# Performance work log

Hardware: AMD Instinct MI355X
Metric: run time of the kernel (lower is better)

The kernel has to match this reference:

```python
import jax, jax.numpy as jnp
import numpy as np

N = 100_000      # total nodes in batched graph
NE = 800_000     # total edges
G = 1_000        # number of graphs in batch
V_DIM = 128      # node feat dim (== H_DIM, required by GRUCell usage)
E_DIM = 64       # edge feat dim
H_DIM = 128      # hidden dim
K_HEAD = 4       # multi-scale interaction heads


def _leaky(x):
    return jnp.where(x >= 0, x, 0.1 * x)


def _gru_cell(x, h, Wih, Whh, bih, bhh):
    # torch nn.GRUCell math; Wih/Whh stored as [in, 3*h] with (r,z,n) chunk order
    gi = x @ Wih + bih
    gh = h @ Whh + bhh
    ir, iz, inn = jnp.split(gi, 3, axis=-1)
    hr, hz, hn = jnp.split(gh, 3, axis=-1)
    r = jax.nn.sigmoid(ir + hr)
    z = jax.nn.sigmoid(iz + hz)
    n = jnp.tanh(inn + r * hn)
    return (1.0 - z) * n + z * h


def setup_inputs() -> dict:
    key = jax.random.key(0)
    ks = iter(jax.random.split(key, 48))
    def rn(shape, scale=0.05):
        return (jax.random.normal(next(ks), shape) * scale).astype(jnp.float32)
    inp = {}
    inp["v"] = rn((N, V_DIM), 1.0)
    inp["e"] = rn((NE, E_DIM), 1.0)
    inp["s"] = rn((G, V_DIM), 1.0)
    inp["edge_src"] = jax.random.randint(next(ks), (NE,), 0, N)
    inp["edge_dst"] = jax.random.randint(next(ks), (NE,), 0, N)
    inp["node_graph"] = jnp.repeat(jnp.arange(G), N // G)  # sorted segment ids
    # top-level linears (stored [in, out])
    inp["A_w"] = rn((V_DIM, H_DIM)); inp["A_b"] = rn((H_DIM,))
    inp["mA_w"] = rn((K_HEAD, V_DIM, H_DIM)); inp["mA_b"] = rn((K_HEAD, H_DIM))
    inp["mB_w"] = rn((K_HEAD, V_DIM, H_DIM)); inp["mB_b"] = rn((K_HEAD, H_DIM))
    inp["mC_w"] = rn((K_HEAD, H_DIM)); inp["mC_b"] = rn((K_HEAD,))
    inp["mD_w"] = rn((K_HEAD, V_DIM, H_DIM)); inp["mD_b"] = rn((K_HEAD, H_DIM))
    inp["B_w"] = rn((H_DIM * K_HEAD, H_DIM)); inp["B_b"] = rn((H_DIM,))
    inp["C_w"] = rn((V_DIM, H_DIM)); inp["C_b"] = rn((H_DIM,))
    inp["K_w"] = rn((E_DIM, H_DIM)); inp["K_b"] = rn((H_DIM,))
    inp["E_w"] = rn((H_DIM + V_DIM, H_DIM)); inp["E_b"] = rn((H_DIM,))
    for pfx in ("gm", "gs"):
        inp[pfx + "_A_w"] = rn((H_DIM, H_DIM)); inp[pfx + "_A_b"] = rn((H_DIM,))
        inp[pfx + "_B_w"] = rn((H_DIM, H_DIM)); inp[pfx + "_B_b"] = rn((H_DIM,))
        inp[pfx + "_Wih"] = rn((H_DIM, 3 * H_DIM)); inp[pfx + "_Whh"] = rn((H_DIM, 3 * H_DIM))
        inp[pfx + "_bih"] = rn((3 * H_DIM,)); inp[pfx + "_bhh"] = rn((3 * H_DIM,))
    return inp


def reference(v, e, s, edge_src, edge_dst, node_graph,
              A_w, A_b, mA_w, mA_b, mB_w, mB_b, mC_w, mC_b, mD_w, mD_b,
              B_w, B_b, C_w, C_b, K_w, K_b, E_w, E_b,
              gm_A_w, gm_A_b, gm_B_w, gm_B_b, gm_Wih, gm_Whh, gm_bih, gm_bhh,
              gs_A_w, gs_A_b, gs_B_w, gs_B_b, gs_Wih, gs_Whh, gs_bih, gs_bhh):
    # super -> super
    s2s = jnp.tanh(s @ A_w + A_b)                                       # [G,H]
    # multi-head node->super attention pooling (Multi_scale_interaction)
    d_node = jnp.tanh(jnp.einsum('nv,kvh->knh', v, mA_w) + mA_b[:, None, :])     # [K,N,H]
    d_super = jnp.tanh(jnp.einsum('gv,kvh->kgh', s, mB_w) + mB_b[:, None, :])    # [K,G,H]
    a = jnp.einsum('knh,kh->nk', d_node * d_super[:, node_graph, :], mC_w) + mC_b[None, :]  # [N,K]
    a_max = jax.ops.segment_max(a, node_graph, num_segments=G, indices_are_sorted=True)
    a_exp = jnp.exp(a - a_max[node_graph])
    denom = jax.ops.segment_sum(a_exp, node_graph, num_segments=G, indices_are_sorted=True)
    attn = a_exp / denom[node_graph]                                    # per-graph softmax, [N,K]
    d_v = jnp.einsum('nv,kvh->nkh', v, mD_w) + mD_b[None, :, :]         # [N,K,H]
    pooled = jax.ops.segment_sum(d_v * attn[:, :, None], node_graph, num_segments=G,
                                 indices_are_sorted=True)               # [G,K,H]
    m2s = jnp.tanh(pooled.reshape(G, K_HEAD * H_DIM) @ B_w + B_b)       # [G,H]
    # super -> node broadcast
    s2m = jnp.tanh(s @ C_w + C_b)[node_graph]                           # [N,H]
    # edge-wise message: leaky_relu(K(e) * v_src) summed into destination node
    ve = _leaky((e @ K_w + K_b) * v[edge_src])                          # [E,H]
    sve = jax.ops.segment_sum(ve, edge_dst, num_segments=N)             # [N,H]
    m2m = _leaky(jnp.concatenate([sve, v], axis=1) @ E_w + E_b)         # [N,H]
    # adaptive GRU gate: node update
    z_m = jax.nn.sigmoid(m2m @ gm_A_w + gm_A_b + s2m @ gm_B_w + gm_B_b)
    h_m = z_m * s2m + (1.0 - z_m) * m2m
    update_v = _gru_cell(v, h_m, gm_Wih, gm_Whh, gm_bih, gm_bhh)
    # adaptive GRU gate: supernode update
    z_s = jax.nn.sigmoid(s2s @ gs_A_w + gs_A_b + m2s @ gs_B_w + gs_B_b)
    h_s = z_s * m2s + (1.0 - z_s) * s2s
    update_s = _gru_cell(s, h_s, gs_Wih, gs_Whh, gs_bih, gs_bhh)
    return (update_v, update_s)
```

## Files before the change

kernel.cpp:

```cpp
#include <hip/hip_runtime.h>

#define NN   100000
#define NEDG 800000
#define NG   1000
#define HD   128
#define EDIM 64

typedef unsigned short u16;
typedef __bf16 bf16x8 __attribute__((ext_vector_type(8)));
typedef float f32x4 __attribute__((ext_vector_type(4)));
typedef u16 u16x8 __attribute__((ext_vector_type(8)));
typedef unsigned u32x4 __attribute__((ext_vector_type(4)));

#define MFMA16(a, b, c) __builtin_amdgcn_mfma_f32_16x16x32_bf16(a, b, c, 0, 0, 0)

#define WS_E    0
#define WS_GA   4096
#define WS_WIH  6144
#define WS_WHH  12288
#define WS_MA0  18432
#define WS_KW   26624
#define WS_LANES 27648

#define BF(base, NTT, ks, nt, lane) \
    (*(const bf16x8*)(wsw + (size_t)((base) + (((ks) * (NTT) + (nt)) * 64 + (lane))) * 8))

__device__ __forceinline__ float sigmoidf_(float x) { return 1.0f / (1.0f + __expf(-x)); }
__device__ __forceinline__ float tanhf_(float x) {
    float ax = fabsf(x);
    float e  = __expf(-2.0f * ax);
    float t  = (1.0f - e) / (1.0f + e);
    return copysignf(t, x);
}
__device__ __forceinline__ float leaky_(float x) { return x >= 0.f ? x : 0.1f * x; }
__device__ __forceinline__ u16 f2bf(float x) {
    union { float f; unsigned u; } c; c.f = x;
    unsigned r = c.u + 0x7FFF + ((c.u >> 16) & 1);
    return (u16)(r >> 16);
}
__device__ __forceinline__ float bfbits2f(unsigned hw) {
    union { unsigned u; float f; } c; c.u = hw << 16; return c.f;
}
__device__ __forceinline__ unsigned pack2bf(float lo, float hi) {
    return (unsigned)f2bf(lo) | ((unsigned)f2bf(hi) << 16);
}
__device__ __forceinline__ bf16x8 mk8(const float* __restrict__ p) {
    float4 a = *(const float4*)p;
    float4 b = *(const float4*)(p + 4);
    union { u32x4 u; bf16x8 v; } c;
    c.u[0] = pack2bf(a.x, a.y);
    c.u[1] = pack2bf(a.z, a.w);
    c.u[2] = pack2bf(b.x, b.y);
    c.u[3] = pack2bf(b.z, b.w);
    return c.v;
}

__device__ __forceinline__ void stg4(u16* lds, int P, int r, int c0, float4 v4) {
    int byteoff = (c0 << 1) ^ ((r & 7) << 4);
    u16* p = lds + r * P + (byteoff >> 1);
    p[0] = f2bf(v4.x); p[1] = f2bf(v4.y); p[2] = f2bf(v4.z); p[3] = f2bf(v4.w);
}
__device__ __forceinline__ void stg1(u16* lds, int P, int r, int c, u16 val) {
    int byteoff = (c << 1) ^ ((r & 7) << 4);
    lds[r * P + (byteoff >> 1)] = val;
}
__device__ __forceinline__ bf16x8 ldA(const u16* lds, int P, int r, int ks, int hi) {
    int byteoff = (ks * 64 + (hi << 4)) ^ ((r & 7) << 4);
    return *(const bf16x8*)(lds + r * P + (byteoff >> 1));
}

__global__ __launch_bounds__(256) void wconv(
    const float* __restrict__ E_w, const float* __restrict__ gmA_w,
    const float* __restrict__ Wih, const float* __restrict__ Whh,
    const float* __restrict__ mA_w, const float* __restrict__ K_w,
    u16* __restrict__ dst)
{
    int t = blockIdx.x * 256 + threadIdx.x;
    if (t >= WS_LANES) return;
    const float* W; int N; int local;
    if (t < 4096)       { W = E_w;  N = 128; local = t; }
    else if (t < 6144)  { W = gmA_w; N = 128; local = t - 4096; }
    else if (t < 12288) { W = Wih;  N = 384; local = t - 6144; }
    else if (t < 18432) { W = Whh;  N = 384; local = t - 12288; }
    else if (t < 26624) { int k = (t - 18432) >> 11; W = mA_w + k * 128 * 128; N = 128; local = (t - 18432) & 2047; }
    else                { W = K_w;  N = 128; local = t - 26624; }
    int lane = local & 63;
    int fid  = local >> 6;
    int NT = N >> 4;
    int ks = fid / NT, nt = fid - ks * NT;
    int krow = ks * 32 + ((lane >> 4) << 3);
    int col  = nt * 16 + (lane & 15);
    u16* d = dst + (size_t)t * 8;
    #pragma unroll
    for (int j = 0; j < 8; j++) d[j] = f2bf(W[(size_t)(krow + j) * N + col]);
}

__global__ __launch_bounds__(256) void k_hist(const int* __restrict__ edst, int* __restrict__ cnt) {
    int i = blockIdx.x * 256 + threadIdx.x;
    if (i < NEDG) atomicAdd(&cnt[edst[i]], 1);
}

__global__ __launch_bounds__(256) void k_scan1(const int* __restrict__ cnt,
                                               int* __restrict__ excl, int* __restrict__ bsum) {
    __shared__ int sd[256];
    int t = threadIdx.x, b = blockIdx.x;
    int base = b * 1024 + t * 4;
    int v0 = (base + 0 < NN) ? cnt[base + 0] : 0;
    int v1 = (base + 1 < NN) ? cnt[base + 1] : 0;
    int v2 = (base + 2 < NN) ? cnt[base + 2] : 0;
    int v3 = (base + 3 < NN) ? cnt[base + 3] : 0;
    int s = v0 + v1 + v2 + v3;
    sd[t] = s;
    __syncthreads();
    for (int off = 1; off < 256; off <<= 1) {
        int x = (t >= off) ? sd[t - off] : 0;
        __syncthreads();
        sd[t] += x;
        __syncthreads();
    }
    int incl = sd[t];
    int ex = incl - s;
    if (base + 0 < NN) excl[base + 0] = ex;
    if (base + 1 < NN) excl[base + 1] = ex + v0;
    if (base + 2 < NN) excl[base + 2] = ex + v0 + v1;
    if (base + 3 < NN) excl[base + 3] = ex + v0 + v1 + v2;
    if (t == 255) bsum[b] = incl;
}

#define NSCB 98
__global__ void k_scan2(int* __restrict__ bsum) {
    if (threadIdx.x == 0 && blockIdx.x == 0) {
        int run = 0;
        for (int i = 0; i < NSCB; i++) { int t = bsum[i]; bsum[i] = run; run += t; }
    }
}

__global__ __launch_bounds__(256) void k_scan3(const int* __restrict__ excl,
                                               const int* __restrict__ bsum,
                                               int* __restrict__ start, int* __restrict__ rowptr) {
    int i = blockIdx.x * 256 + threadIdx.x;
    if (i < NN) {
        int sv = excl[i] + bsum[i >> 10];
        start[i] = sv;
        rowptr[i] = sv;
    }
    if (i == NN) rowptr[NN] = NEDG;
}

__global__ __launch_bounds__(256) void k_scatter(const int* __restrict__ edst,
                                                 int* __restrict__ start,
                                                 int* __restrict__ perm,
                                                 int* __restrict__ outpos) {
    int i = blockIdx.x * 256 + threadIdx.x;
    if (i < NEDG) {
        int pos = atomicAdd(&start[edst[i]], 1);
        perm[pos] = i;
        outpos[i] = pos;
    }
}

__global__ __launch_bounds__(128) void k1_graph(
    const float* __restrict__ s,
    const float* __restrict__ A_w, const float* __restrict__ A_b,
    const float* __restrict__ mB_w, const float* __restrict__ mB_b,
    const float* __restrict__ mC_w,
    const float* __restrict__ C_w, const float* __restrict__ C_b,
    const float* __restrict__ gmB_w, const float* __restrict__ gmA_b, const float* __restrict__ gmB_b,
    float* __restrict__ s2s, float* __restrict__ wkg,
    float* __restrict__ s2m_tab, float* __restrict__ t2)
{
    __shared__ float sm[HD];
    __shared__ float sm2[HD];
    const int g = blockIdx.x, t = threadIdx.x;
    sm[t] = s[g * HD + t];
    __syncthreads();
    {
        float a = 0.f;
        #pragma unroll 8
        for (int i = 0; i < HD; i++) a = fmaf(sm[i], A_w[i * HD + t], a);
        s2s[g * HD + t] = tanhf_(a + A_b[t]);
    }
    for (int k = 0; k < 4; k++) {
        float a = 0.f;
        const float* W = mB_w + k * HD * HD;
        #pragma unroll 8
        for (int i = 0; i < HD; i++) a = fmaf(sm[i], W[i * HD + t], a);
        float d = tanhf_(a + mB_b[k * HD + t]);
        wkg[(k * NG + g) * HD + t] = d * mC_w[k * HD + t];
    }
    float s2m;
    {
        float a = 0.f;
        #pragma unroll 8
        for (int i = 0; i < HD; i++) a = fmaf(sm[i], C_w[i * HD + t], a);
        s2m = tanhf_(a + C_b[t]);
        s2m_tab[g * HD + t] = s2m;
    }
    sm2[t] = s2m;
    __syncthreads();
    {
        float a = 0.f;
        #pragma unroll 8
        for (int i = 0; i < HD; i++) a = fmaf(sm2[i], gmB_w[i * HD + t], a);
        t2[g * HD + t] = a + gmA_b[t] + gmB_b[t];
    }
}

__global__ __launch_bounds__(256) void k2_ascore(
    const float* __restrict__ v, const int* __restrict__ ngr,
    const u16* __restrict__ wsw,
    const float* __restrict__ mA_b, const float* __restrict__ mC_b,
    const float* __restrict__ wkg,
    float* __restrict__ aexp, float* __restrict__ denom)
{
    __shared__ u16 VT[64 * 128];
    const int tid = threadIdx.x;
    const int n0 = blockIdx.x * 64;
    #pragma unroll
    for (int l = 0; l < 8; l++) {
        int i = tid + 256 * l;
        int r = i >> 5, c0 = (i & 31) << 2;
        int node = n0 + r;
        float4 vv = (node < NN) ? *(const float4*)(v + (size_t)node * HD + c0)
                                : make_float4(0.f, 0.f, 0.f, 0.f);
        stg4(VT, 128, r, c0, vv);
    }
    __syncthreads();
    const int lane = tid & 63, w = tid >> 6;
    const int l15 = lane & 15, hi = lane >> 4;
    const int rbase = w * 16;
    bf16x8 av[4];
    #pragma unroll
    for (int ks = 0; ks < 4; ks++) av[ks] = ldA(VT, 128, rbase + l15, ks, hi);
    int gq[4], nodeq[4];
    #pragma unroll
    for (int q = 0; q < 4; q++) {
        int nd = n0 + rbase + hi * 4 + q;
        nodeq[q] = nd;
        gq[q] = ngr[min(nd, NN - 1)];
    }
    for (int k = 0; k < 4; k++) {
        float rs[4] = {0.f, 0.f, 0.f, 0.f};
        const float* bias = mA_b + k * HD;
        #pragma unroll
        for (int nt = 0; nt < 8; nt++) {
            f32x4 acc = {0.f, 0.f, 0.f, 0.f};
            #pragma unroll
            for (int ks = 0; ks < 4; ks++)
                acc = MFMA16(av[ks], BF(WS_MA0 + k * 2048, 8, ks, nt, lane), acc);
            int col = nt * 16 + l15;
            float bb = bias[col];
            #pragma unroll
            for (int q = 0; q < 4; q++)
                rs[q] += tanhf_(acc[q] + bb) * wkg[((size_t)k * NG + gq[q]) * HD + col];
        }
        #pragma unroll
        for (int q = 0; q < 4; q++) {
            float x = rs[q];
            x += __shfl_xor(x, 1); x += __shfl_xor(x, 2);
            x += __shfl_xor(x, 4); x += __shfl_xor(x, 8);
            if (l15 == 0 && nodeq[q] < NN) {
                float ev = __expf(x + mC_b[k]);
                aexp[(size_t)nodeq[q] * 4 + k] = ev;
                atomicAdd(&denom[gq[q] * 4 + k], ev);
            }
        }
    }
}

__global__ __launch_bounds__(256) void k3a_edge(
    const float* __restrict__ e, const float* __restrict__ v,
    const int* __restrict__ esrc, const int* __restrict__ outpos,
    const u16* __restrict__ wsw, const float* __restrict__ K_b,
    u16* __restrict__ vesrt)
{
    __shared__ u16 ET[64 * 64];
    __shared__ u16 OUT[64 * 128];
    __shared__ int posa[64];
    const int tid = threadIdx.x;
    const int e0 = blockIdx.x * 64;
    if (tid < 64) posa[tid] = outpos[e0 + tid];
    #pragma unroll
    for (int l = 0; l < 4; l++) {
        int i = tid + 256 * l;
        int r = i >> 4, c0 = (i & 15) << 2;
        float4 ev4 = *(const float4*)(e + (size_t)(e0 + r) * EDIM + c0);
        stg4(ET, 64, r, c0, ev4);
    }
    __syncthreads();
    const int lane = tid & 63, w = tid >> 6;
    const int l15 = lane & 15, hi = lane >> 4;
    const int rbase = w * 16;
    bf16x8 ae[2];
    #pragma unroll
    for (int ks = 0; ks < 2; ks++) ae[ks] = ldA(ET, 64, rbase + l15, ks, hi);
    int sq[4];
    #pragma unroll
    for (int q = 0; q < 4; q++) sq[q] = esrc[e0 + rbase + hi * 4 + q];
    #pragma unroll
    for (int nt = 0; nt < 8; nt++) {
        f32x4 acc = {0.f, 0.f, 0.f, 0.f};
        acc = MFMA16(ae[0], BF(WS_KW, 8, 0, nt, lane), acc);
        acc = MFMA16(ae[1], BF(WS_KW, 8, 1, nt, lane), acc);
        int col = nt * 16 + l15;
        float kb = K_b[col];
        #pragma unroll
        for (int q = 0; q < 4; q++) {
            float val = leaky_((acc[q] + kb) * v[(size_t)sq[q] * HD + col]);
            stg1(OUT, 128, rbase + hi * 4 + q, col, f2bf(val));
        }
    }
    __syncthreads();
    #pragma unroll
    for (int l = 0; l < 4; l++) {
        int i = tid + 256 * l;
        int r = i >> 4, seg = i & 15;
        int segp = seg ^ (r & 7);
        u16x8 val = *(const u16x8*)&OUT[r * 128 + segp * 8];
        *(u16x8*)(vesrt + (size_t)posa[r] * HD + ((segp ^ (r & 7)) * 8)) = val;
    }
}

__global__ __launch_bounds__(256) void k3b_segsum(
    const u16* __restrict__ vesrt, const int* __restrict__ rowptr,
    float* __restrict__ sve)
{
    const int wid = threadIdx.x >> 6, lane = threadIdx.x & 63;
    const int n = blockIdx.x * 4 + wid;
    if (n >= NN) return;
    const int r0 = rowptr[n], r1 = rowptr[n + 1];
    const unsigned* base = (const unsigned*)vesrt;
    float a0 = 0.f, a1 = 0.f;
    int r = r0;
    for (; r + 4 <= r1; r += 4) {
        unsigned x0 = base[(size_t)(r + 0) * 64 + lane];
        unsigned x1 = base[(size_t)(r + 1) * 64 + lane];
        unsigned x2 = base[(size_t)(r + 2) * 64 + lane];
        unsigned x3 = base[(size_t)(r + 3) * 64 + lane];
        a0 += bfbits2f(x0 & 0xffff) + bfbits2f(x1 & 0xffff) + bfbits2f(x2 & 0xffff) + bfbits2f(x3 & 0xffff);
        a1 += bfbits2f(x0 >> 16) + bfbits2f(x1 >> 16) + bfbits2f(x2 >> 16) + bfbits2f(x3 >> 16);
    }
    for (; r < r1; r++) {
        unsigned x = base[(size_t)r * 64 + lane];
        a0 += bfbits2f(x & 0xffff);
        a1 += bfbits2f(x >> 16);
    }
    *(float2*)(sve + (size_t)n * HD + lane * 2) = make_float2(a0, a1);
}

__global__ __launch_bounds__(256) void k3_edge_sorted(
    const float* __restrict__ e, const float* __restrict__ v,
    const int* __restrict__ esrc, const int* __restrict__ edst,
    const int* __restrict__ perm,
    const u16* __restrict__ wsw, const float* __restrict__ K_b,
    float* __restrict__ sve)
{
    __shared__ u16 ET[64 * 64];
    __shared__ int pid[64];
    const int tid = threadIdx.x;
    const int e0 = blockIdx.x * 64;
    if (tid < 64) pid[tid] = perm[e0 + tid];
    __syncthreads();
    #pragma unroll
    for (int l = 0; l < 4; l++) {
        int i = tid + 256 * l;
        int r = i >> 4, c0 = (i & 15) << 2;
        float4 ev4 = *(const float4*)(e + (size_t)pid[r] * EDIM + c0);
        stg4(ET, 64, r, c0, ev4);
    }
    __syncthreads();
    const int lane = tid & 63, w = tid >> 6;
    const int l15 = lane & 15, hi = lane >> 4;
    const int rbase = w * 16;
    bf16x8 ae[2];
    #pragma unroll
    for (int ks = 0; ks < 2; ks++) ae[ks] = ldA(ET, 64, rbase + l15, ks, hi);
    int sq[4], dq[4];
    #pragma unroll
    for (int q = 0; q < 4; q++) {
        int ei = pid[rbase + hi * 4 + q];
        sq[q] = esrc[ei]; dq[q] = edst[ei];
    }
    #pragma unroll
    for (int nt = 0; nt < 8; nt++) {
        f32x4 acc = {0.f, 0.f, 0.f, 0.f};
        acc = MFMA16(ae[0], BF(WS_KW, 8, 0, nt, lane), acc);
        acc = MFMA16(ae[1], BF(WS_KW, 8, 1, nt, lane), acc);
        int col = nt * 16 + l15;
        float kb = K_b[col];
        float vals[4];
        #pragma unroll
        for (int q = 0; q < 4; q++)
            vals[q] = leaky_((acc[q] + kb) * v[(size_t)sq[q] * HD + col]);
        float a = vals[0];
        #pragma unroll
        for (int q = 1; q < 4; q++) {
            if (dq[q] == dq[q - 1]) a += vals[q];
            else { atomicAdd(&sve[(size_t)dq[q - 1] * HD + col], a); a = vals[q]; }
        }
        atomicAdd(&sve[(size_t)dq[3] * HD + col], a);
    }
}

__global__ __launch_bounds__(256) void k3_edge_unsorted(
    const float* __restrict__ e, const float* __restrict__ v,
    const int* __restrict__ esrc, const int* __restrict__ edst,
    const u16* __restrict__ wsw, const float* __restrict__ K_b,
    float* __restrict__ sve)
{
    __shared__ u16 ET[64 * 64];
    const int tid = threadIdx.x;
    const int e0 = blockIdx.x * 64;
    #pragma unroll
    for (int l = 0; l < 4; l++) {
        int i = tid + 256 * l;
        int r = i >> 4, c0 = (i & 15) << 2;
        float4 ev4 = *(const float4*)(e + (size_t)(e0 + r) * EDIM + c0);
        stg4(ET, 64, r, c0, ev4);
    }
    __syncthreads();
    const int lane = tid & 63, w = tid >> 6;
    const int l15 = lane & 15, hi = lane >> 4;
    const int rbase = w * 16;
    bf16x8 ae[2];
    #pragma unroll
    for (int ks = 0; ks < 2; ks++) ae[ks] = ldA(ET, 64, rbase + l15, ks, hi);
    int sq[4], dq[4];
    #pragma unroll
    for (int q = 0; q < 4; q++) {
        int ei = e0 + rbase + hi * 4 + q;
        sq[q] = esrc[ei]; dq[q] = edst[ei];
    }
    #pragma unroll
    for (int nt = 0; nt < 8; nt++) {
        f32x4 acc = {0.f, 0.f, 0.f, 0.f};
        acc = MFMA16(ae[0], BF(WS_KW, 8, 0, nt, lane), acc);
        acc = MFMA16(ae[1], BF(WS_KW, 8, 1, nt, lane), acc);
        int col = nt * 16 + l15;
        float kb = K_b[col];
        #pragma unroll
        for (int q = 0; q < 4; q++) {
            float val = leaky_((acc[q] + kb) * v[(size_t)sq[q] * HD + col]);
            atomicAdd(&sve[(size_t)dq[q] * HD + col], val);
        }
    }
}

__global__ __launch_bounds__(256) void k4_vbar(
    const float* __restrict__ v, const int* __restrict__ ngr,
    const float* __restrict__ aexp, const float* __restrict__ denom,
    float* __restrict__ vbar)
{
    const int tid = threadIdx.x;
    const int d = tid & 127;
    const int hf = tid >> 7;
    const int n0 = blockIdx.x * 32 + hf * 16;
    int gcur = -1;
    float a0 = 0.f, a1 = 0.f, a2 = 0.f, a3 = 0.f;
    float4 rd = make_float4(0.f, 0.f, 0.f, 0.f);
    for (int nd = 0; nd < 16; nd++) {
        int n = n0 + nd;
        int g = ngr[n];
        if (g != gcur) {
            if (gcur >= 0) {
                atomicAdd(&vbar[(gcur * 4 + 0) * HD + d], a0);
                atomicAdd(&vbar[(gcur * 4 + 1) * HD + d], a1);
                atomicAdd(&vbar[(gcur * 4 + 2) * HD + d], a2);
                atomicAdd(&vbar[(gcur * 4 + 3) * HD + d], a3);
                a0 = a1 = a2 = a3 = 0.f;
            }
            float4 dn = *(const float4*)&denom[g * 4];
            rd = make_float4(1.f / dn.x, 1.f / dn.y, 1.f / dn.z, 1.f / dn.w);
            gcur = g;
        }
        float4 ae = *(const float4*)&aexp[n * 4];
        float vv = v[(size_t)n * HD + d];
        a0 = fmaf(ae.x * rd.x, vv, a0);
        a1 = fmaf(ae.y * rd.y, vv, a1);
        a2 = fmaf(ae.z * rd.z, vv, a2);
        a3 = fmaf(ae.w * rd.w, vv, a3);
    }
    atomicAdd(&vbar[(gcur * 4 + 0) * HD + d], a0);
    atomicAdd(&vbar[(gcur * 4 + 1) * HD + d], a1);
    atomicAdd(&vbar[(gcur * 4 + 2) * HD + d], a2);
    atomicAdd(&vbar[(gcur * 4 + 3) * HD + d], a3);
}

__global__ __launch_bounds__(128) void k5_super(
    const float* __restrict__ s, const float* __restrict__ vbar,
    const float* __restrict__ mD_w, const float* __restrict__ mD_b,
    const float* __restrict__ B_w, const float* __restrict__ B_b,
    const float* __restrict__ s2s,
    const float* __restrict__ gsA_w, const float* __restrict__ gsA_b,
    const float* __restrict__ gsB_w, const float* __restrict__ gsB_b,
    const float* __restrict__ gsWih, const float* __restrict__ gsWhh,
    const float* __restrict__ gsbih, const float* __restrict__ gsbhh,
    float* __restrict__ out_s)
{
    __shared__ float vb[4 * HD];
    __shared__ float p[4 * HD];
    __shared__ float m2s_l[HD];
    __shared__ float s2s_l[HD];
    __shared__ float hs_l[HD];
    __shared__ float srow[HD];
    const int g = blockIdx.x, t = threadIdx.x;
    #pragma unroll
    for (int l = 0; l < 4; l++) vb[t + HD * l] = vbar[(size_t)g * 4 * HD + t + HD * l];
    srow[t]  = s[g * HD + t];
    s2s_l[t] = s2s[g * HD + t];
    __syncthreads();
    for (int k = 0; k < 4; k++) {
        float a = 0.f;
        const float* W = mD_w + k * HD * HD;
        #pragma unroll 8
        for (int i = 0; i < HD; i++) a = fmaf(vb[k * HD + i], W[i * HD + t], a);
        p[k * HD + t] = a + mD_b[k * HD + t];
    }
    __syncthreads();
    float m2s;
    {
        float a = 0.f;
        #pragma unroll 8
        for (int j = 0; j < 4 * HD; j++) a = fmaf(p[j], B_w[j * HD + t], a);
        m2s = tanhf_(a + B_b[t]);
        m2s_l[t] = m2s;
    }
    __syncthreads();
    float hs;
    {
        float za = 0.f, zb = 0.f;
        #pragma unroll 8
        for (int i = 0; i < HD; i++) {
            za = fmaf(s2s_l[i], gsA_w[i * HD + t], za);
            zb = fmaf(m2s_l[i], gsB_w[i * HD + t], zb);
        }
        float z = sigmoidf_(za + gsA_b[t] + zb + gsB_b[t]);
        hs = z * m2s + (1.f - z) * s2s_l[t];
        hs_l[t] = hs;
    }
    __syncthreads();
    float gi0 = 0.f, gh0 = 0.f, gi1 = 0.f, gh1 = 0.f, gi2 = 0.f, gh2 = 0.f;
    #pragma unroll 4
    for (int i = 0; i < HD; i++) {
        float sv = srow[i], hv = hs_l[i];
        gi0 = fmaf(sv, gsWih[i * 384 + t], gi0);
        gh0 = fmaf(hv, gsWhh[i * 384 + t], gh0);
        gi1 = fmaf(sv, gsWih[i * 384 + 128 + t], gi1);
        gh1 = fmaf(hv, gsWhh[i * 384 + 128 + t], gh1);
        gi2 = fmaf(sv, gsWih[i * 384 + 256 + t], gi2);
        gh2 = fmaf(hv, gsWhh[i * 384 + 256 + t], gh2);
    }
    float r  = sigmoidf_(gi0 + gsbih[t] + gh0 + gsbhh[t]);
    float z2 = sigmoidf_(gi1 + gsbih[128 + t] + gh1 + gsbhh[128 + t]);
    float nn = tanhf_(gi2 + gsbih[256 + t] + r * (gh2 + gsbhh[256 + t]));
    out_s[g * HD + t] = (1.f - z2) * nn + z2 * hs;
}

__global__ __launch_bounds__(256) void k6_node(
    const float* __restrict__ v, const int* __restrict__ ngr,
    const float* __restrict__ sve, const u16* __restrict__ wsw,
    const float* __restrict__ E_b,
    const float* __restrict__ s2m_tab, const float* __restrict__ t2,
    const float* __restrict__ bih, const float* __restrict__ bhh,
    float* __restrict__ out_v)
{
    __shared__ u16 TT[4][16 * 128];
    const int tid = threadIdx.x;
    const int lane = tid & 63, w = tid >> 6;
    const int l15 = lane & 15, hi = lane >> 4;
    const int n0 = blockIdx.x * 64 + w * 16;
    u16* T = TT[w];
    const int arow = min(n0 + l15, NN - 1);
    bf16x8 av[4], ax[4];
    #pragma unroll
    for (int ks = 0; ks < 4; ks++) {
        av[ks] = mk8(v   + (size_t)arow * HD + ks * 32 + hi * 8);
        ax[ks] = mk8(sve + (size_t)arow * HD + ks * 32 + hi * 8);
    }
    int gq[4], nodeq[4];
    #pragma unroll
    for (int q = 0; q < 4; q++) {
        int nd = n0 + hi * 4 + q;
        nodeq[q] = nd;
        gq[q] = ngr[min(nd, NN - 1)];
    }
    f32x4 hmf[8];
    #pragma unroll
    for (int nt = 0; nt < 8; nt++) {
        f32x4 acc = {0.f, 0.f, 0.f, 0.f};
        #pragma unroll
        for (int ks = 0; ks < 4; ks++) acc = MFMA16(ax[ks], BF(WS_E, 8, ks, nt, lane), acc);
        #pragma unroll
        for (int ks = 0; ks < 4; ks++) acc = MFMA16(av[ks], BF(WS_E, 8, 4 + ks, nt, lane), acc);
        float eb = E_b[nt * 16 + l15];
        #pragma unroll
        for (int q = 0; q < 4; q++) hmf[nt][q] = leaky_(acc[q] + eb);
    }
    #pragma unroll
    for (int nt = 0; nt < 8; nt++) {
        int col = nt * 16 + l15;
        #pragma unroll
        for (int q = 0; q < 4; q++) stg1(T, 128, hi * 4 + q, col, f2bf(hmf[nt][q]));
    }
    bf16x8 am[4];
    #pragma unroll
    for (int ks = 0; ks < 4; ks++) am[ks] = ldA(T, 128, l15, ks, hi);
    #pragma unroll
    for (int nt = 0; nt < 8; nt++) {
        f32x4 acc = {0.f, 0.f, 0.f, 0.f};
        #pragma unroll
        for (int ks = 0; ks < 4; ks++) acc = MFMA16(am[ks], BF(WS_GA, 8, ks, nt, lane), acc);
        int col = nt * 16 + l15;
        #pragma unroll
        for (int q = 0; q < 4; q++) {
            int g = gq[q];
            float z  = sigmoidf_(acc[q] + t2[(size_t)g * HD + col]);
            hmf[nt][q] = z * s2m_tab[(size_t)g * HD + col] + (1.f - z) * hmf[nt][q];
        }
    }
    #pragma unroll
    for (int nt = 0; nt < 8; nt++) {
        int col = nt * 16 + l15;
        #pragma unroll
        for (int q = 0; q < 4; q++) stg1(T, 128, hi * 4 + q, col, f2bf(hmf[nt][q]));
    }
    bf16x8 ah[4];
    #pragma unroll
    for (int ks = 0; ks < 4; ks++) ah[ks] = ldA(T, 128, l15, ks, hi);
    #pragma unroll
    for (int nt = 0; nt < 8; nt++) {
        f32x4 air = {0.f,0.f,0.f,0.f}, aiz = {0.f,0.f,0.f,0.f}, ain = {0.f,0.f,0.f,0.f};
        f32x4 ahr = {0.f,0.f,0.f,0.f}, ahz = {0.f,0.f,0.f,0.f}, ahn = {0.f,0.f,0.f,0.f};
        #pragma unroll
        for (int ks = 0; ks < 4; ks++) {
            air = MFMA16(av[ks], BF(WS_WIH, 24, ks, nt,      lane), air);
            ahr = MFMA16(ah[ks], BF(WS_WHH, 24, ks, nt,      lane), ahr);
            aiz = MFMA16(av[ks], BF(WS_WIH, 24, ks, nt + 8,  lane), aiz);
            ahz = MFMA16(ah[ks], BF(WS_WHH, 24, ks, nt + 8,  lane), ahz);
            ain = MFMA16(av[ks], BF(WS_WIH, 24, ks, nt + 16, lane), ain);
            ahn = MFMA16(ah[ks], BF(WS_WHH, 24, ks, nt + 16, lane), ahn);
        }
        int col = nt * 16 + l15;
        float br  = bih[col] + bhh[col];
        float bz  = bih[HD + col] + bhh[HD + col];
        float bi3 = bih[2 * HD + col];
        float bh3 = bhh[2 * HD + col];
        #pragma unroll
        for (int q = 0; q < 4; q++) {
            float r   = sigmoidf_(air[q] + ahr[q] + br);
            float z   = sigmoidf_(aiz[q] + ahz[q] + bz);
            float nnv = tanhf_(ain[q] + bi3 + r * (ahn[q] + bh3));
            if (nodeq[q] < NN)
                out_v[(size_t)nodeq[q] * HD + col] = (1.f - z) * nnv + z * hmf[nt][q];
        }
    }
}

extern "C" void kernel_launch(void* const* d_in, const int* in_sizes, int n_in,
                              void* d_out, int out_size, void* d_ws, size_t ws_size,
                              hipStream_t stream)
{
    const float* v    = (const float*)d_in[0];
    const float* e    = (const float*)d_in[1];
    const float* s    = (const float*)d_in[2];
    const int*   esrc = (const int*)d_in[3];
    const int*   edst = (const int*)d_in[4];
    const int*   ngr  = (const int*)d_in[5];
    const float* A_w  = (const float*)d_in[6];
    const float* A_b  = (const float*)d_in[7];
    const float* mA_w = (const float*)d_in[8];
    const float* mA_b = (const float*)d_in[9];
    const float* mB_w = (const float*)d_in[10];
    const float* mB_b = (const float*)d_in[11];
    const float* mC_w = (const float*)d_in[12];
    const float* mC_b = (const float*)d_in[13];
    const float* mD_w = (const float*)d_in[14];
    const float* mD_b = (const float*)d_in[15];
    const float* B_w  = (const float*)d_in[16];
    const float* B_b  = (const float*)d_in[17];
    const float* C_w  = (const float*)d_in[18];
    const float* C_b  = (const float*)d_in[19];
    const float* K_w  = (const float*)d_in[20];
    const float* K_b  = (const float*)d_in[21];
    const float* E_w  = (const float*)d_in[22];
    const float* E_b  = (const float*)d_in[23];
    const float* gmA_w = (const float*)d_in[24];
    const float* gmA_b = (const float*)d_in[25];
    const float* gmB_w = (const float*)d_in[26];
    const float* gmB_b = (const float*)d_in[27];
    const float* gmWih = (const float*)d_in[28];
    const float* gmWhh = (const float*)d_in[29];
    const float* gmbih = (const float*)d_in[30];
    const float* gmbhh = (const float*)d_in[31];
    const float* gsA_w = (const float*)d_in[32];
    const float* gsA_b = (const float*)d_in[33];
    const float* gsB_w = (const float*)d_in[34];
    const float* gsB_b = (const float*)d_in[35];
    const float* gsWih = (const float*)d_in[36];
    const float* gsWhh = (const float*)d_in[37];
    const float* gsbih = (const float*)d_in[38];
    const float* gsbhh = (const float*)d_in[39];

    float* ws      = (float*)d_ws;
    float* sve     = ws;
    float* aexp    = sve + 12800000;
    float* denom   = aexp + 400000;
    float* wkg     = denom + 4000;
    float* s2s     = wkg + 512000;
    float* s2m_tab = s2s + 128000;
    float* t2      = s2m_tab + 128000;
    float* vbar    = t2 + 128000;
    u16*   wswz    = (u16*)(vbar + 512000);
    int*   isc     = (int*)(wswz + 221184);
    int*   cnt     = isc;
    int*   excl    = cnt + 100000;
    int*   bsum    = excl + 100000;
    int*   startp  = bsum + 128;
    int*   rowptr  = startp + 100000;
    int*   perm    = rowptr + 100032;
    int*   outpos  = perm + 800000;
    u16*   vesrt   = (u16*)(outpos + 800000);
    const size_t NEED_SORT = ((size_t)((int*)vesrt - (int*)d_ws)) * 4;
    const size_t NEED_FULL = NEED_SORT + (size_t)102400000 * 2;
    const bool do_sort = ws_size >= NEED_SORT;
    const bool do_full = ws_size >= NEED_FULL;

    hipMemsetAsync(denom, 0, (size_t)4000 * 4, stream);
    hipMemsetAsync(vbar, 0, (size_t)512000 * 4, stream);
    if (!do_full) hipMemsetAsync(sve, 0, (size_t)12800000 * 4, stream);

    float* out_v = (float*)d_out;
    float* out_s = out_v + (size_t)NN * HD;

    wconv<<<(WS_LANES + 255) / 256, 256, 0, stream>>>(E_w, gmA_w, gmWih, gmWhh, mA_w, K_w, wswz);
    k1_graph<<<NG, 128, 0, stream>>>(s, A_w, A_b, mB_w, mB_b, mC_w, C_w, C_b,
                                     gmB_w, gmA_b, gmB_b, s2s, wkg, s2m_tab, t2);
    if (do_sort) {
        hipMemsetAsync(cnt, 0, (size_t)100000 * 4, stream);
        k_hist<<<(NEDG + 255) / 256, 256, 0, stream>>>(edst, cnt);
        k_scan1<<<NSCB, 256, 0, stream>>>(cnt, excl, bsum);
        k_scan2<<<1, 64, 0, stream>>>(bsum);
        k_scan3<<<(NN + 256) / 256, 256, 0, stream>>>(excl, bsum, startp, rowptr);
        k_scatter<<<(NEDG + 255) / 256, 256, 0, stream>>>(edst, startp, perm, outpos);
    }
    k2_ascore<<<(NN + 63) / 64, 256, 0, stream>>>(v, ngr, wswz, mA_b, mC_b, wkg, aexp, denom);
    if (do_full) {
        k3a_edge<<<NEDG / 64, 256, 0, stream>>>(e, v, esrc, outpos, wswz, K_b, vesrt);
        k3b_segsum<<<(NN + 3) / 4, 256, 0, stream>>>(vesrt, rowptr, sve);
    } else if (do_sort) {
        k3_edge_sorted<<<NEDG / 64, 256, 0, stream>>>(e, v, esrc, edst, perm, wswz, K_b, sve);
    } else {
        k3_edge_unsorted<<<NEDG / 64, 256, 0, stream>>>(e, v, esrc, edst, wswz, K_b, sve);
    }
    k4_vbar<<<NN / 32, 256, 0, stream>>>(v, ngr, aexp, denom, vbar);
    k5_super<<<NG, 128, 0, stream>>>(s, vbar, mD_w, mD_b, B_w, B_b, s2s,
                                     gsA_w, gsA_b, gsB_w, gsB_b,
                                     gsWih, gsWhh, gsbih, gsbhh, out_s);
    k6_node<<<(NN + 63) / 64, 256, 0, stream>>>(v, ngr, sve, wswz, E_b, s2m_tab, t2,
                                                gmbih, gmbhh, out_v);
}
```

Baseline: 739.0 us.

## Fuse CSR segment-sum of edge messages into node GRU kernel

In the sorted-edge path, the per-node segment sum over bf16 edge messages now runs inside the node update kernel, which writes the sums straight into LDS as the MFMA A operand. This removes the separate segsum kernel and the fp32 sve round trip through global memory. The cost is that each wave loops serially over its 16 nodes, which may unbalance work and lengthen the node kernel. The node kernel is also moved earlier in the launch order, before vbar and the supernode kernel.

```diff
diff --git a/kernel.cpp b/kernel.cpp
--- a/kernel.cpp
+++ b/kernel.cpp
@@ -63,6 +63,10 @@
 __device__ __forceinline__ void stg1(u16* lds, int P, int r, int c, u16 val) {
     int byteoff = (c << 1) ^ ((r & 7) << 4);
     lds[r * P + (byteoff >> 1)] = val;
+}
+__device__ __forceinline__ void stgu32(u16* lds, int P, int r, int cpair, unsigned val) {
+    int byteoff = (cpair << 2) ^ ((r & 7) << 4);
+    *(unsigned*)(lds + r * P + (byteoff >> 1)) = val;
 }
 __device__ __forceinline__ bf16x8 ldA(const u16* lds, int P, int r, int ks, int hi) {
     int byteoff = (ks * 64 + (hi << 4)) ^ ((r & 7) << 4);
@@ -556,7 +560,131 @@
     out_s[g * HD + t] = (1.f - z2) * nn + z2 * hs;
 }
 
-__global__ __launch_bounds__(256) void k6_node(
+__global__ __launch_bounds__(256) void k6_fused(
+    const float* __restrict__ v, const int* __restrict__ ngr,
+    const u16* __restrict__ vesrt, const int* __restrict__ rowptr,
+    const u16* __restrict__ wsw,
+    const float* __restrict__ E_b,
+    const float* __restrict__ s2m_tab, const float* __restrict__ t2,
+    const float* __restrict__ bih, const float* __restrict__ bhh,
+    float* __restrict__ out_v)
+{
+    __shared__ u16 TT[4][16 * 128];
+    const int tid = threadIdx.x;
+    const int lane = tid & 63, w = tid >> 6;
+    const int l15 = lane & 15, hi = lane >> 4;
+    const int n0 = blockIdx.x * 64 + w * 16;
+    u16* T = TT[w];
+    const int arow = min(n0 + l15, NN - 1);
+    bf16x8 av[4];
+    #pragma unroll
+    for (int ks = 0; ks < 4; ks++) av[ks] = mk8(v + (size_t)arow * HD + ks * 32 + hi * 8);
+    const unsigned* vb = (const unsigned*)vesrt;
+    for (int i = 0; i < 16; i++) {
+        int n = min(n0 + i, NN - 1);
+        int r0 = rowptr[n], r1 = rowptr[n + 1];
+        float a0 = 0.f, a1 = 0.f;
+        int r = r0;
+        for (; r + 4 <= r1; r += 4) {
+            unsigned x0 = vb[(size_t)(r + 0) * 64 + lane];
+            unsigned x1 = vb[(size_t)(r + 1) * 64 + lane];
+            unsigned x2 = vb[(size_t)(r + 2) * 64 + lane];
+            unsigned x3 = vb[(size_t)(r + 3) * 64 + lane];
+            a0 += bfbits2f(x0 & 0xffff) + bfbits2f(x1 & 0xffff) + bfbits2f(x2 & 0xffff) + bfbits2f(x3 & 0xffff);
+            a1 += bfbits2f(x0 >> 16) + bfbits2f(x1 >> 16) + bfbits2f(x2 >> 16) + bfbits2f(x3 >> 16);
+        }
+        for (; r < r1; r++) {
+            unsigned x = vb[(size_t)r * 64 + lane];
+            a0 += bfbits2f(x & 0xffff);
+            a1 += bfbits2f(x >> 16);
+        }
+        stgu32(T, 128, i, lane, pack2bf(a0, a1));
+    }
+    bf16x8 ax[4];
+    #pragma unroll
+    for (int ks = 0; ks < 4; ks++) ax[ks] = ldA(T, 128, l15, ks, hi);
+    int gq[4], nodeq[4];
+    #pragma unroll
+    for (int q = 0; q < 4; q++) {
+        int nd = n0 + hi * 4 + q;
+        nodeq[q] = nd;
+        gq[q] = ngr[min(nd, NN - 1)];
+    }
+    f32x4 m2m[8];
+    #pragma unroll
+    for (int nt = 0; nt < 8; nt++) {
+        f32x4 acc = {0.f, 0.f, 0.f, 0.f};
+        #pragma unroll
+        for (int ks = 0; ks < 4; ks++) acc = MFMA16(ax[ks], BF(WS_E, 8, ks, nt, lane), acc);
+        #pragma unroll
+        for (int ks = 0; ks < 4; ks++) acc = MFMA16(av[ks], BF(WS_E, 8, 4 + ks, nt, lane), acc);
+        float eb = E_b[nt * 16 + l15];
+        #pragma unroll
+        for (int q = 0; q < 4; q++) m2m[nt][q] = leaky_(acc[q] + eb);
+    }
+    #pragma unroll
+    for (int nt = 0; nt < 8; nt++) {
+        int col = nt * 16 + l15;
+        #pragma unroll
+        for (int q = 0; q < 4; q++) stg1(T, 128, hi * 4 + q, col, f2bf(m2m[nt][q]));
+    }
+    bf16x8 am[4];
+    #pragma unroll
+    for (int ks = 0; ks < 4; ks++) am[ks] = ldA(T, 128, l15, ks, hi);
+    unsigned hmp[8][2];
+    #pragma unroll
+    for (int nt = 0; nt < 8; nt++) {
+        f32x4 acc = {0.f, 0.f, 0.f, 0.f};
+        #pragma unroll
+        for (int ks = 0; ks < 4; ks++) acc = MFMA16(am[ks], BF(WS_GA, 8, ks, nt, lane), acc);
+        int col = nt * 16 + l15;
+        float hm[4];
+        #pragma unroll
+        for (int q = 0; q < 4; q++) {
+            int g = gq[q];
+            float z = sigmoidf_(acc[q] + t2[(size_t)g * HD + col]);
+            hm[q] = z * s2m_tab[(size_t)g * HD + col] + (1.f - z) * m2m[nt][q];
+        }
+        hmp[nt][0] = pack2bf(hm[0], hm[1]);
+        hmp[nt][1] = pack2bf(hm[2], hm[3]);
+        #pragma unroll
+        for (int q = 0; q < 4; q++) stg1(T, 128, hi * 4 + q, col, f2bf(hm[q]));
+    }
+    bf16x8 ah[4];
+    #pragma unroll
+    for (int ks = 0; ks < 4; ks++) ah[ks] = ldA(T, 128, l15, ks, hi);
+    #pragma unroll
+    for (int nt = 0; nt < 8; nt++) {
+        f32x4 air = {0.f,0.f,0.f,0.f}, aiz = {0.f,0.f,0.f,0.f}, ain = {0.f,0.f,0.f,0.f};
+        f32x4 ahr = {0.f,0.f,0.f,0.f}, ahz = {0.f,0.f,0.f,0.f}, ahn = {0.f,0.f,0.f,0.f};
+        #pragma unroll
+        for (int ks = 0; ks < 4; ks++) {
+            air = MFMA16(av[ks], BF(WS_WIH, 24, ks, nt,      lane), air);
+            ahr = MFMA16(ah[ks], BF(WS_WHH, 24, ks, nt,      lane), ahr);
+            aiz = MFMA16(av[ks], BF(WS_WIH, 24, ks, nt + 8,  lane), aiz);
+            ahz = MFMA16(ah[ks], BF(WS_WHH, 24, ks, nt + 8,  lane), ahz);
+            ain = MFMA16(av[ks], BF(WS_WIH, 24, ks, nt + 16, lane), ain);
+            ahn = MFMA16(ah[ks], BF(WS_WHH, 24, ks, nt + 16, lane), ahn);
+        }
+        int col = nt * 16 + l15;
+        float br  = bih[col] + bhh[col];
+        float bz  = bih[HD + col] + bhh[HD + col];
+        float bi3 = bih[2 * HD + col];
+        float bh3 = bhh[2 * HD + col];
+        float hmq[4] = { bfbits2f(hmp[nt][0] & 0xffff), bfbits2f(hmp[nt][0] >> 16),
+                         bfbits2f(hmp[nt][1] & 0xffff), bfbits2f(hmp[nt][1] >> 16) };
+        #pragma unroll
+        for (int q = 0; q < 4; q++) {
+            float r   = sigmoidf_(air[q] + ahr[q] + br);
+            float z   = sigmoidf_(aiz[q] + ahz[q] + bz);
+            float nnv = tanhf_(ain[q] + bi3 + r * (ahn[q] + bh3));
+            if (nodeq[q] < NN)
+                out_v[(size_t)nodeq[q] * HD + col] = (1.f - z) * nnv + z * hmq[q];
+        }
+    }
+}
+
+__global__ __launch_bounds__(256) void k6_node_sve(
     const float* __restrict__ v, const int* __restrict__ ngr,
     const float* __restrict__ sve, const u16* __restrict__ wsw,
     const float* __restrict__ E_b,
@@ -746,16 +874,19 @@
     k2_ascore<<<(NN + 63) / 64, 256, 0, stream>>>(v, ngr, wswz, mA_b, mC_b, wkg, aexp, denom);
     if (do_full) {
         k3a_edge<<<NEDG / 64, 256, 0, stream>>>(e, v, esrc, outpos, wswz, K_b, vesrt);
-        k3b_segsum<<<(NN + 3) / 4, 256, 0, stream>>>(vesrt, rowptr, sve);
-    } else if (do_sort) {
-        k3_edge_sorted<<<NEDG / 64, 256, 0, stream>>>(e, v, esrc, edst, perm, wswz, K_b, sve);
+        k6_fused<<<(NN + 63) / 64, 256, 0, stream>>>(v, ngr, vesrt, rowptr, wswz, E_b,
+                                                     s2m_tab, t2, gmbih, gmbhh, out_v);
     } else {
-        k3_edge_unsorted<<<NEDG / 64, 256, 0, stream>>>(e, v, esrc, edst, wswz, K_b, sve);
+        if (do_sort) {
+            k3_edge_sorted<<<NEDG / 64, 256, 0, stream>>>(e, v, esrc, edst, perm, wswz, K_b, sve);
+        } else {
+            k3_edge_unsorted<<<NEDG / 64, 256, 0, stream>>>(e, v, esrc, edst, wswz, K_b, sve);
+        }
+        k6_node_sve<<<(NN + 63) / 64, 256, 0, stream>>>(v, ngr, sve, wswz, E_b, s2m_tab, t2,
+                                                        gmbih, gmbhh, out_v);
     }
     k4_vbar<<<NN / 32, 256, 0, stream>>>(v, ngr, aexp, denom, vbar);
     k5_super<<<NG, 128, 0, stream>>>(s, vbar, mD_w, mD_b, B_w, B_b, s2s,
                                      gsA_w, gsA_b, gsB_w, gsB_b,
                                      gsWih, gsWhh, gsbih, gsbhh, out_s);
-    k6_node<<<(NN + 63) / 64, 256, 0, stream>>>(v, ngr, sve, wswz, E_b, s2m_tab, t2,
-                                                gmbih, gmbhh, out_v);
-}
+}
```

New measurement: 795.6 us. 1.08x slower.
